# Optimization experiments

Hardware: AMD Instinct MI355X
Metric: run time of the kernel (lower is better)

The kernel has to match this reference:

```python
import jax, jax.numpy as jnp
import numpy as np

ROWS, COLS = 10, 4
B, N = 65536, 16


def setup_inputs() -> dict:
    key = jax.random.key(0)
    kx, kc = jax.random.split(key)
    # 0.5 scale keeps trace(x^(rows+1))^cols finite in float32 (spectral radius ~2)
    x = jax.random.normal(kx, (B, N, N), dtype=jnp.float32) * 0.5
    # kaiming_normal_ on a 2D (rows, cols) tensor: std = sqrt(2 / fan_in), fan_in = cols
    coef = jax.random.normal(kc, (ROWS, COLS), dtype=jnp.float32) * np.float32(np.sqrt(2.0 / COLS))
    return {"x": x, "coef": coef}


def reference(x, coef):
    # x: [B, N, N]; coef: [rows, cols]
    rows, cols = coef.shape
    n = x.shape[-1] * x.shape[-2]  # numel per sample

    A0 = jnp.matmul(x, x)  # x^2, the first a_series entry

    def step(A, _):
        # original records trace(a_series[i]) = trace(x^(i+2)), then advances the power
        tr = jnp.trace(A, axis1=-2, axis2=-1)  # [B]
        return jnp.matmul(x, A), tr

    _, traces = jax.lax.scan(step, A0, None, length=rows)  # traces: [rows, B]
    t = traces.T  # [B, rows]

    jexp = jnp.arange(1, cols + 1, dtype=jnp.float32)  # j+1 exponents
    iexp = jnp.arange(rows, dtype=jnp.float32)
    # feature[b, i, j] = trace(x^(i+2))^(j+1) / n^(i+j+1)
    denom = jnp.float32(n) ** (iexp[:, None] + jexp[None, :])  # [rows, cols]
    feats = (t[:, :, None] ** jexp[None, None, :]) / denom  # [B, rows, cols]

    # terms = coef * feats, summed over (rows, cols) per sample -> [B]
    return jnp.einsum('rc,brc->b', coef, feats)
```

## Files before the change

### kernel.cpp

```cpp
#include <hip/hip_runtime.h>

typedef __fp16 f16x4 __attribute__((ext_vector_type(4)));
typedef __fp16 f16x2 __attribute__((ext_vector_type(2)));
typedef float f32x4 __attribute__((ext_vector_type(4)));

__device__ __forceinline__ f16x4 cat(f16x2 lo, f16x2 hi) {
    return __builtin_shufflevector(lo, hi, 0, 1, 2, 3);
}
__device__ __forceinline__ f16x2 u2h(unsigned v) {
    union { unsigned u; f16x2 h; } x; x.u = v; return x.h;
}
template <int CTRL>
__device__ __forceinline__ float dpp_add(float v) {
    int s = __builtin_amdgcn_update_dpp(0, __float_as_int(v), CTRL, 0xf, 0xf, true);
    return v + __int_as_float(s);
}

__global__ __launch_bounds__(256, 6) void acoef_kernel(
    const float* __restrict__ x,
    const float* __restrict__ coef,
    float* __restrict__ out)
{
    const int lane = threadIdx.x & 63;
    const int b = (blockIdx.x * 256 + (int)threadIdx.x) >> 6;

    const int n = lane & 15;
    const int q = lane >> 4;
    const bool diagsel = ((n >> 2) == q);

    const float4 a = *(const float4*)(x + (size_t)b * 256 + n * 16 + 4 * q);

    unsigned ilo = 0, ihi = 0;
    if (diagsel) {
        ilo = ((n & 3) == 0 ? 0x3C00u : 0u) | ((n & 3) == 1 ? 0x3C000000u : 0u);
        ihi = ((n & 3) == 2 ? 0x3C00u : 0u) | ((n & 3) == 3 ? 0x3C000000u : 0u);
    }
    const f16x4 idB = cat(u2h(ilo), u2h(ihi));
    unsigned slo = (n == 0 ? 0x3C00u : 0u) | (n == 1 ? 0x3C000000u : 0u);
    unsigned shi = (n == 2 ? 0x3C00u : 0u) | (n == 3 ? 0x3C000000u : 0u);
    const f16x4 selB  = cat(u2h(slo), u2h(shi));
    const f16x4 onesA = cat(u2h(0x3C003C00u), u2h(0x3C003C00u));
    const f32x4 zero  = {0.f, 0.f, 0.f, 0.f};

    float4 cf[3]; float scl[3];
    #pragma unroll
    for (int p = 0; p < 3; ++p) {
        int s = 4 * p + n;
        int idx = s > 9 ? 9 : s;
        cf[p]  = *(const float4*)(coef + 4 * idx);
        scl[p] = __int_as_float((127 - 8 * s) << 23);
    }

    f16x4 xA = cat(__builtin_amdgcn_cvt_pkrtz(a.x, a.y),
                   __builtin_amdgcn_cvt_pkrtz(a.z, a.w));
    f32x4 d = __builtin_amdgcn_mfma_f32_16x16x16f16(xA, idB, zero, 0, 0, 0);
    f16x4 xB = cat(__builtin_amdgcn_cvt_pkrtz(d[0], d[1]),
                   __builtin_amdgcn_cvt_pkrtz(d[2], d[3]));

    f32x4 acc = __builtin_amdgcn_mfma_f32_16x16x16f16(xA, xB, zero, 0, 0, 0);

    f16x2 prpk[6];
    float trf = 0.0f;
    #pragma unroll
    for (int st = 0; st < 10; ++st) {
        float sA = (n & 1) ? acc[1] : acc[0];
        float sB = (n & 1) ? acc[3] : acc[2];
        float dv = (n & 2) ? sB : sA;
        float tr = diagsel ? dv : 0.0f;
        if (st & 1) prpk[st >> 1] = __builtin_amdgcn_cvt_pkrtz(trf, tr);
        else        trf = tr;

        if (st < 9) {
            f16x4 bf = cat(__builtin_amdgcn_cvt_pkrtz(acc[0], acc[1]),
                           __builtin_amdgcn_cvt_pkrtz(acc[2], acc[3]));
            acc = __builtin_amdgcn_mfma_f32_16x16x16f16(xA, bf, zero, 0, 0, 0);
        }
    }
    prpk[5] = u2h(0u);

    float result = 0.0f;
    #pragma unroll
    for (int p = 0; p < 3; ++p) {
        f16x4 Ap = cat(prpk[2 * p], prpk[2 * p + 1]);
        f32x4 c1 = __builtin_amdgcn_mfma_f32_16x16x16f16(Ap, selB, zero, 0, 0, 0);
        f16x4 Bp = cat(__builtin_amdgcn_cvt_pkrtz(c1[0], c1[1]),
                       __builtin_amdgcn_cvt_pkrtz(c1[2], c1[3]));
        f32x4 c2 = __builtin_amdgcn_mfma_f32_16x16x16f16(onesA, Bp, zero, 0, 0, 0);
        float t = c2[0];
        float sv = t * 0x1p-8f;
        float h = fmaf(sv, cf[p].w, cf[p].z);
        h = fmaf(sv, h, cf[p].y);
        h = fmaf(sv, h, cf[p].x);
        result = fmaf(sv * h, scl[p], result);
    }
    result = dpp_add<0xB1>(result);
    result = dpp_add<0x4E>(result);
    if (lane == 0) out[b] = result;
}

extern "C" void kernel_launch(void* const* d_in, const int* in_sizes, int n_in,
                              void* d_out, int out_size, void* d_ws, size_t ws_size,
                              hipStream_t stream) {
    const float* x    = (const float*)d_in[0];
    const float* coef = (const float*)d_in[1];
    float* out        = (float*)d_out;
    const int B = in_sizes[0] / 256;
    acoef_kernel<<<dim3(B / 4), dim3(256), 0, stream>>>(x, coef, out);
}
```

Before: 97.13 us.

## Make kernel persistent with double-buffered async global-to-LDS staging

Replaces the one-sample-per-wave launch with a fixed grid of 1024 blocks. Each wave walks through its block's slice two samples at a time. The next pair of 16x16 matrices is staged into a per-wave double buffer in LDS with global_load_lds, and an explicit vmcnt wait lets the loads overlap the MFMA power chain of the current pair. This aims to hide global-load latency and cut launch and wave-startup overhead. In exchange it lowers the number of resident waves, leaves the dependent MFMA chains less latency hiding, and assumes B divides evenly by 1024*8.

```diff
diff --git a/kernel.cpp b/kernel.cpp
--- a/kernel.cpp
+++ b/kernel.cpp
@@ -16,19 +16,29 @@
     return v + __int_as_float(s);
 }
 
-__global__ __launch_bounds__(256, 6) void acoef_kernel(
+__device__ __forceinline__ void stage16(const float* g, float* l) {
+    __builtin_amdgcn_global_load_lds(
+        (const __attribute__((address_space(1))) void*)g,
+        (__attribute__((address_space(3))) void*)l, 16, 0, 0);
+}
+
+__global__ __launch_bounds__(256) void acoef_kernel(
     const float* __restrict__ x,
     const float* __restrict__ coef,
-    float* __restrict__ out)
+    float* __restrict__ out,
+    int B)
 {
+    __shared__ float smem[4096];
+
     const int lane = threadIdx.x & 63;
-    const int b = (blockIdx.x * 256 + (int)threadIdx.x) >> 6;
-
+    const int w    = threadIdx.x >> 6;
     const int n = lane & 15;
     const int q = lane >> 4;
     const bool diagsel = ((n >> 2) == q);
 
-    const float4 a = *(const float4*)(x + (size_t)b * 256 + n * 16 + 4 * q);
+    const int SPB  = B / gridDim.x;
+    const int base = blockIdx.x * SPB;
+    const int NT   = SPB / 8;
 
     unsigned ilo = 0, ihi = 0;
     if (diagsel) {
@@ -51,51 +61,77 @@
         scl[p] = __int_as_float((127 - 8 * s) << 23);
     }
 
-    f16x4 xA = cat(__builtin_amdgcn_cvt_pkrtz(a.x, a.y),
-                   __builtin_amdgcn_cvt_pkrtz(a.z, a.w));
-    f32x4 d = __builtin_amdgcn_mfma_f32_16x16x16f16(xA, idB, zero, 0, 0, 0);
-    f16x4 xB = cat(__builtin_amdgcn_cvt_pkrtz(d[0], d[1]),
-                   __builtin_amdgcn_cvt_pkrtz(d[2], d[3]));
+    float* lw = smem + w * 1024;
 
-    f32x4 acc = __builtin_amdgcn_mfma_f32_16x16x16f16(xA, xB, zero, 0, 0, 0);
+    {
+        const float* g = x + (size_t)(base + 2 * w) * 256 + lane * 4;
+        stage16(g,       lw);
+        stage16(g + 256, lw + 256);
+    }
 
-    f16x2 prpk[6];
-    float trf = 0.0f;
-    #pragma unroll
-    for (int st = 0; st < 10; ++st) {
-        float sA = (n & 1) ? acc[1] : acc[0];
-        float sB = (n & 1) ? acc[3] : acc[2];
-        float dv = (n & 2) ? sB : sA;
-        float tr = diagsel ? dv : 0.0f;
-        if (st & 1) prpk[st >> 1] = __builtin_amdgcn_cvt_pkrtz(trf, tr);
-        else        trf = tr;
+    #pragma unroll 1
+    for (int t = 0; t < NT; ++t) {
+        const int tn = (t + 1 < NT) ? t + 1 : t;
+        const int bc = (t & 1) * 512;
+        const int bn = (~t & 1) * 512;
 
-        if (st < 9) {
-            f16x4 bf = cat(__builtin_amdgcn_cvt_pkrtz(acc[0], acc[1]),
-                           __builtin_amdgcn_cvt_pkrtz(acc[2], acc[3]));
-            acc = __builtin_amdgcn_mfma_f32_16x16x16f16(xA, bf, zero, 0, 0, 0);
+        const float* g = x + (size_t)(base + tn * 8 + 2 * w) * 256 + lane * 4;
+        stage16(g,       lw + bn);
+        stage16(g + 256, lw + bn + 256);
+
+        asm volatile("s_waitcnt vmcnt(2)" ::: "memory");
+
+        #pragma unroll
+        for (int c = 0; c < 2; ++c) {
+            const float4 a = *(const float4*)(lw + bc + c * 256 + n * 16 + q * 4);
+
+            f16x4 xA = cat(__builtin_amdgcn_cvt_pkrtz(a.x, a.y),
+                           __builtin_amdgcn_cvt_pkrtz(a.z, a.w));
+            f32x4 d = __builtin_amdgcn_mfma_f32_16x16x16f16(xA, idB, zero, 0, 0, 0);
+            f16x4 xB = cat(__builtin_amdgcn_cvt_pkrtz(d[0], d[1]),
+                           __builtin_amdgcn_cvt_pkrtz(d[2], d[3]));
+
+            f32x4 acc = __builtin_amdgcn_mfma_f32_16x16x16f16(xA, xB, zero, 0, 0, 0);
+
+            f16x2 prpk[6];
+            float trf = 0.0f;
+            #pragma unroll
+            for (int st = 0; st < 10; ++st) {
+                float sA = (n & 1) ? acc[1] : acc[0];
+                float sB = (n & 1) ? acc[3] : acc[2];
+                float dv = (n & 2) ? sB : sA;
+                float tr = diagsel ? dv : 0.0f;
+                if (st & 1) prpk[st >> 1] = __builtin_amdgcn_cvt_pkrtz(trf, tr);
+                else        trf = tr;
+
+                if (st < 9) {
+                    f16x4 bf = cat(__builtin_amdgcn_cvt_pkrtz(acc[0], acc[1]),
+                                   __builtin_amdgcn_cvt_pkrtz(acc[2], acc[3]));
+                    acc = __builtin_amdgcn_mfma_f32_16x16x16f16(xA, bf, zero, 0, 0, 0);
+                }
+            }
+            prpk[5] = u2h(0u);
+
+            float result = 0.0f;
+            #pragma unroll
+            for (int p = 0; p < 3; ++p) {
+                f16x4 Ap = cat(prpk[2 * p], prpk[2 * p + 1]);
+                f32x4 c1 = __builtin_amdgcn_mfma_f32_16x16x16f16(Ap, selB, zero, 0, 0, 0);
+                f16x4 Bp = cat(__builtin_amdgcn_cvt_pkrtz(c1[0], c1[1]),
+                               __builtin_amdgcn_cvt_pkrtz(c1[2], c1[3]));
+                f32x4 c2 = __builtin_amdgcn_mfma_f32_16x16x16f16(onesA, Bp, zero, 0, 0, 0);
+                float t2 = c2[0];
+                float sv = t2 * 0x1p-8f;
+                float h = fmaf(sv, cf[p].w, cf[p].z);
+                h = fmaf(sv, h, cf[p].y);
+                h = fmaf(sv, h, cf[p].x);
+                result = fmaf(sv * h, scl[p], result);
+            }
+            result = dpp_add<0xB1>(result);
+            result = dpp_add<0x4E>(result);
+            if (lane == 0) out[base + t * 8 + 2 * w + c] = result;
         }
     }
-    prpk[5] = u2h(0u);
-
-    float result = 0.0f;
-    #pragma unroll
-    for (int p = 0; p < 3; ++p) {
-        f16x4 Ap = cat(prpk[2 * p], prpk[2 * p + 1]);
-        f32x4 c1 = __builtin_amdgcn_mfma_f32_16x16x16f16(Ap, selB, zero, 0, 0, 0);
-        f16x4 Bp = cat(__builtin_amdgcn_cvt_pkrtz(c1[0], c1[1]),
-                       __builtin_amdgcn_cvt_pkrtz(c1[2], c1[3]));
-        f32x4 c2 = __builtin_amdgcn_mfma_f32_16x16x16f16(onesA, Bp, zero, 0, 0, 0);
-        float t = c2[0];
-        float sv = t * 0x1p-8f;
-        float h = fmaf(sv, cf[p].w, cf[p].z);
-        h = fmaf(sv, h, cf[p].y);
-        h = fmaf(sv, h, cf[p].x);
-        result = fmaf(sv * h, scl[p], result);
-    }
-    result = dpp_add<0xB1>(result);
-    result = dpp_add<0x4E>(result);
-    if (lane == 0) out[b] = result;
 }
 
 extern "C" void kernel_launch(void* const* d_in, const int* in_sizes, int n_in,
@@ -105,5 +141,5 @@
     const float* coef = (const float*)d_in[1];
     float* out        = (float*)d_out;
     const int B = in_sizes[0] / 256;
-    acoef_kernel<<<dim3(B / 4), dim3(256), 0, stream>>>(x, coef, out);
+    acoef_kernel<<<dim3(1024), dim3(256), 0, stream>>>(x, coef, out, B);
 }
```

After: 102.6 us. 5.6% more time.
